# Kernel optimization log

Measured on AMD Instinct MI355X. Metric: run time of the kernel, lower is better.

## Reference

```python
import jax, jax.numpy as jnp
import numpy as np


def setup_inputs() -> dict:
    key = jax.random.key(0)
    k1, k2, k3 = jax.random.split(key, 3)
    b, c, h, w = 4, 124, 64, 64
    x = jax.random.normal(k1, (b, c, h, w), dtype=jnp.float32)
    # 1x1 conv, no bias -> channel-mixing matrix [c_out, c_in]
    Wb = jax.random.normal(k2, (c, c), dtype=jnp.float32) * (1.0 / np.sqrt(c))
    gamma = jax.random.normal(k3, (1,), dtype=jnp.float32) * 0.1
    return {"x": x, "Wb": Wb, "gamma": gamma}


def reference(x, Wb, gamma):
    b, c, h, w = x.shape
    n = h * w
    xf = x.reshape(b, c, n)                      # [b, c, n]
    # NOTE: original code applies convB for B, C, and D (convC/convD unused)
    Bf = jnp.einsum('oc,bcn->bon', Wb, xf)       # [b, c, n]
    # S = softmax(B^T C, dim=last) -> [b, n, n]
    scores = jnp.einsum('bcm,bcn->bmn', Bf, Bf)
    S = jax.nn.softmax(scores, axis=2)
    # E = D @ S^T -> E[b,c,m] = sum_n D[b,c,n] * S[b,m,n]
    E = jnp.einsum('bcn,bmn->bcm', Bf, S).reshape(b, c, h, w)
    return gamma[0] * E + x
```

## Files before the change

kernel.cpp:

```cpp
#include <hip/hip_runtime.h>

typedef short short8 __attribute__((ext_vector_type(8)));
typedef short short4v __attribute__((ext_vector_type(4)));
typedef float floatx4 __attribute__((ext_vector_type(4)));

#define BB 4
#define CC 124
#define CP 128
#define NN 4096
#define NGRP 256
#define NG32 128
#define NSPLIT 4
#define KSPLIT (NN / NSPLIT)
#define TN 32
#define NCHUNK (KSPLIT / TN)
#define NBUF 4

static __device__ __forceinline__ unsigned short f2bf_fast(float f) {
    return (unsigned short)((__float_as_uint(f) + 0x8000u) >> 16);
}
static __device__ __forceinline__ float bf2f(unsigned short u) {
    return __uint_as_float(((unsigned int)u) << 16);
}
static __device__ __forceinline__ unsigned int pkbf(float a, float b) {
    unsigned int ua = __float_as_uint(a) + 0x8000u;
    unsigned int ub = __float_as_uint(b) + 0x8000u;
    return __builtin_amdgcn_perm(ub, ua, 0x07060302u);
}
union PK2 { short4v s; unsigned int u[2]; };
union PK8 { short8 s; unsigned int u[4]; };

#if defined(__has_builtin) && __has_builtin(__builtin_amdgcn_exp2f)
static __device__ __forceinline__ float exp2_raw(float x) {
    return __builtin_amdgcn_exp2f(x);
}
#else
static __device__ __forceinline__ float exp2_raw(float x) {
    float r;
    asm("v_exp_f32 %0, %1\n\ts_nop 0" : "=v"(r) : "v"(x));
    return r;
}
#endif

static __device__ __forceinline__ void gl16(const unsigned short* g, unsigned short* l) {
    __builtin_amdgcn_global_load_lds(
        (const __attribute__((address_space(1))) unsigned int*)g,
        (__attribute__((address_space(3))) unsigned int*)l, 16, 0, 0);
}

__global__ __launch_bounds__(256) void wtrans_kernel(const float* __restrict__ Wb,
                                                     unsigned short* __restrict__ wbt) {
    __shared__ float ws[32][125];
    const int blk = blockIdx.x;
    const int tid = threadIdx.x;
    for (int i = tid; i < 32 * CC; i += 256) {
        int ol = i / CC, c = i - ol * CC;
        int o = blk * 32 + ol;
        ws[ol][c] = (o < CC) ? Wb[o * CC + c] : 0.f;
    }
    __syncthreads();
    for (int i = tid; i < CC * 32; i += 256) {
        int c = i >> 5, ol = i & 31;
        wbt[c * CP + blk * 32 + ol] = f2bf_fast(ws[ol][c]);
    }
}

__global__ __launch_bounds__(256, 4) void bf_proj_kernel(const float* __restrict__ x,
                                                         const unsigned short* __restrict__ wbt,
                                                         unsigned short* __restrict__ kfrag,
                                                         unsigned short* __restrict__ vfrag,
                                                         float* __restrict__ m2) {
    __shared__ __align__(16) float xs[CC][36];
    __shared__ float msh[32][33];
    const int tid = threadIdx.x;
    const int b = blockIdx.y;
    const int n0 = blockIdx.x * 32;
    const float* xb = x + (size_t)b * CC * NN + n0;
    for (int i = tid; i < CC * 8; i += 256) {
        int c = i >> 3, nq = i & 7;
        *(floatx4*)&xs[c][nq * 4] = *(const floatx4*)(xb + (size_t)c * NN + nq * 4);
    }
    __syncthreads();
    const int og = tid >> 3;
    const int nidx = tid & 7;
    const int o0 = og * 4;
    float acc[4][4];
#pragma unroll
    for (int k = 0; k < 4; ++k)
#pragma unroll
        for (int j = 0; j < 4; ++j) acc[k][j] = 0.f;
    for (int c = 0; c < CC; ++c) {
        floatx4 xv = *(const floatx4*)&xs[c][nidx * 4];
        short4v wv = *(const short4v*)&wbt[c * CP + o0];
#pragma unroll
        for (int k = 0; k < 4; ++k) {
            float wf = bf2f((unsigned short)wv[k]);
            acc[k][0] += wf * xv[0];
            acc[k][1] += wf * xv[1];
            acc[k][2] += wf * xv[2];
            acc[k][3] += wf * xv[3];
        }
    }
    float sq[4] = {0.f, 0.f, 0.f, 0.f};
#pragma unroll
    for (int k = 0; k < 4; ++k)
#pragma unroll
        for (int j = 0; j < 4; ++j) sq[j] += acc[k][j] * acc[k][j];
#pragma unroll
    for (int j = 0; j < 4; ++j) msh[og][nidx * 4 + j] = sq[j];
    const int g16 = (n0 >> 4) + (nidx & 1);
    const int tK = o0 >> 5;
    const int qK = (o0 >> 3) & 3;
    const int halfo = o0 & 7;
#pragma unroll
    for (int j = 0; j < 4; ++j) {
        PK2 kv;
        kv.u[0] = pkbf(acc[0][j], acc[1][j]);
        kv.u[1] = pkbf(acc[2][j], acc[3][j]);
        int row16 = 4 * (nidx >> 1) + j;
        size_t unit = ((size_t)(b * NGRP + g16) * 4 + tK) * 64 + qK * 16 + row16;
        *(short4v*)&kfrag[unit * 8 + halfo] = kv.s;
    }
    const int g32 = n0 >> 5;
    const int quadn = nidx >> 1;
    const int halfn = (nidx & 1) * 4;
#pragma unroll
    for (int k = 0; k < 4; ++k) {
        int c = o0 + k;
        PK2 vv;
        if (c == 124) {
            vv.u[0] = 0x3f803f80u;
            vv.u[1] = 0x3f803f80u;
        } else {
            vv.u[0] = pkbf(acc[k][0], acc[k][1]);
            vv.u[1] = pkbf(acc[k][2], acc[k][3]);
        }
        size_t unit = ((size_t)(b * NG32 + g32) * 8 + (c >> 4)) * 64 + quadn * 16 + (c & 15);
        *(short4v*)&vfrag[unit * 8 + halfn] = vv.s;
    }
    __syncthreads();
    if (tid < 32) {
        float s = 0.f;
#pragma unroll
        for (int og2 = 0; og2 < 32; ++og2) s += msh[og2][tid];
        m2[(size_t)b * NN + n0 + tid] = s * 1.44269504088896340736f;
    }
}

__global__ __launch_bounds__(256, 2) void attn_kernel(const unsigned short* __restrict__ kfrag,
                                                      const unsigned short* __restrict__ vfrag,
                                                      const float* __restrict__ m2,
                                                      unsigned short* __restrict__ opart) {
    __shared__ __align__(16) unsigned short kbuf[NBUF][8 * 512];
    __shared__ __align__(16) unsigned short vbuf[NBUF][8 * 512];
    const int id = blockIdx.x;
    const int ghi = id & 7;
    const int r_ = id >> 3;
    const int mtile = r_ & 31;
    const int glo = r_ >> 5;
    const int grp = ghi * 2 + glo;
    const int b = grp & 3;
    const int split = grp >> 2;
    const int w = threadIdx.x >> 6;
    const int lane = threadIdx.x & 63;
    const int col = lane & 15;
    const int quad = lane >> 4;
    const int m0 = mtile * 128 + w * 32;
    const floatx4 fzero = {0.f, 0.f, 0.f, 0.f};
    const float L2E = 1.44269504088896340736f;

    short8 qf[2][4];
#pragma unroll
    for (int ms = 0; ms < 2; ++ms) {
        const int gq = (m0 >> 4) + ms;
#pragma unroll
        for (int t = 0; t < 4; ++t)
            qf[ms][t] = *(const short8*)&kfrag[((size_t)(b * NGRP + gq) * 4 + t) * 512 + lane * 8];
    }
    const int mq = 8 * (col >> 2) + (col & 3);
    float nmreg[2];
    nmreg[0] = -m2[(size_t)b * NN + m0 + mq];
    nmreg[1] = -m2[(size_t)b * NN + m0 + mq + 4];

    floatx4 oacc[2][8];
#pragma unroll
    for (int ms = 0; ms < 2; ++ms)
#pragma unroll
        for (int s8 = 0; s8 < 8; ++s8) oacc[ms][s8] = fzero;

    auto stage = [&](int ch, int sel) {
        if (w < 2) {
            const int g16b = split * (KSPLIT >> 4) + ch * 2;
#pragma unroll
            for (int i = 0; i < 4; ++i) {
                int p = w * 4 + i;
                const unsigned short* src =
                    kfrag + ((size_t)(b * NGRP + g16b + (p >> 2)) * 4 + (p & 3)) * 512 + lane * 8;
                gl16(src, &kbuf[sel][p * 512]);
            }
        } else {
            const int g32b = split * (KSPLIT >> 5) + ch;
#pragma unroll
            for (int i = 0; i < 4; ++i) {
                int q = (w - 2) * 4 + i;
                const unsigned short* src =
                    vfrag + ((size_t)(b * NG32 + g32b) * 8 + q) * 512 + lane * 8;
                gl16(src, &vbuf[sel][q * 512]);
            }
        }
    };

    stage(0, 0);
    stage(1, 1);
    stage(2, 2);
    for (int ch = 0; ch < NCHUNK; ++ch) {
        if (ch + 2 < NCHUNK)      asm volatile("s_waitcnt vmcnt(8)" ::: "memory");
        else if (ch + 1 < NCHUNK) asm volatile("s_waitcnt vmcnt(4)" ::: "memory");
        else                      asm volatile("s_waitcnt vmcnt(0)" ::: "memory");
        __builtin_amdgcn_s_barrier();
        asm volatile("" ::: "memory");
        if (ch + 3 < NCHUNK) stage(ch + 3, (ch + 3) & (NBUF - 1));
        const int sel = ch & (NBUF - 1);
        floatx4 st[2][2];
#pragma unroll
        for (int ms = 0; ms < 2; ++ms)
#pragma unroll
            for (int u = 0; u < 2; ++u) st[ms][u] = fzero;
#pragma unroll
        for (int t = 0; t < 4; ++t) {
#pragma unroll
            for (int u = 0; u < 2; ++u) {
                short8 kf = *(const short8*)&kbuf[sel][((u * 4 + t) * 64 + lane) * 8];
                st[0][u] = __builtin_amdgcn_mfma_f32_16x16x32_bf16(kf, qf[0][t], st[0][u], 0, 0, 0);
                st[1][u] = __builtin_amdgcn_mfma_f32_16x16x32_bf16(kf, qf[1][t], st[1][u], 0, 0, 0);
            }
        }
        float ev[2][2][4];
#pragma unroll
        for (int ms = 0; ms < 2; ++ms)
#pragma unroll
            for (int u = 0; u < 2; ++u)
#pragma unroll
                for (int r = 0; r < 4; ++r)
                    ev[ms][u][r] = exp2_raw(__builtin_fmaf(st[ms][u][r], L2E, nmreg[ms]));
        PK8 af[2];
#pragma unroll
        for (int ms = 0; ms < 2; ++ms) {
            af[ms].u[0] = pkbf(ev[ms][0][0], ev[ms][0][1]);
            af[ms].u[1] = pkbf(ev[ms][0][2], ev[ms][0][3]);
            af[ms].u[2] = pkbf(ev[ms][1][0], ev[ms][1][1]);
            af[ms].u[3] = pkbf(ev[ms][1][2], ev[ms][1][3]);
        }
#pragma unroll
        for (int s8 = 0; s8 < 8; ++s8) {
            short8 vf = *(const short8*)&vbuf[sel][(s8 * 64 + lane) * 8];
            oacc[0][s8] = __builtin_amdgcn_mfma_f32_16x16x32_bf16(af[0].s, vf, oacc[0][s8], 0, 0, 0);
            oacc[1][s8] = __builtin_amdgcn_mfma_f32_16x16x32_bf16(af[1].s, vf, oacc[1][s8], 0, 0, 0);
        }
    }
    unsigned short* ob = opart + (size_t)(split * BB + b) * NN * CP;
#pragma unroll
    for (int ms = 0; ms < 2; ++ms)
#pragma unroll
        for (int s8 = 0; s8 < 8; ++s8)
#pragma unroll
            for (int r = 0; r < 4; ++r)
                ob[(size_t)(m0 + 8 * quad + 4 * ms + r) * CP + s8 * 16 + col] = f2bf_fast(oacc[ms][s8][r]);
}

__global__ __launch_bounds__(256) void combine_kernel(const unsigned short* __restrict__ opart,
                                                      const float* __restrict__ x,
                                                      const float* __restrict__ gamma,
                                                      float* __restrict__ out) {
    __shared__ float es[32 * 133];
    __shared__ float Lsh[32];
    const int t = threadIdx.x;
    const int b = blockIdx.y;
    const int m0 = blockIdx.x * 32;
    if (t < 32) {
        float L = 0.f;
#pragma unroll
        for (int s = 0; s < NSPLIT; ++s)
            L += bf2f(opart[((size_t)(s * BB + b) * NN + m0 + t) * CP + 124]);
        Lsh[t] = gamma[0] / L;
    }
    const int tc = t & 31, tm = t >> 5;
    float acc[4][4];
#pragma unroll
    for (int i = 0; i < 4; ++i)
#pragma unroll
        for (int j = 0; j < 4; ++j) acc[i][j] = 0.f;
    for (int s = 0; s < NSPLIT; ++s) {
        const unsigned short* obp = opart + ((size_t)(s * BB + b) * NN + m0 + tm * 4) * CP + tc * 4;
#pragma unroll
        for (int i = 0; i < 4; ++i) {
            short4v v = *(const short4v*)(obp + (size_t)i * CP);
            acc[i][0] += bf2f((unsigned short)v[0]);
            acc[i][1] += bf2f((unsigned short)v[1]);
            acc[i][2] += bf2f((unsigned short)v[2]);
            acc[i][3] += bf2f((unsigned short)v[3]);
        }
    }
#pragma unroll
    for (int i = 0; i < 4; ++i)
#pragma unroll
        for (int j = 0; j < 4; ++j) es[(tm * 4 + i) * 133 + tc * 4 + j] = acc[i][j];
    __syncthreads();
    const int wave = t >> 6, lane = t & 63;
    const int half = lane >> 5, lm = lane & 31;
#pragma unroll
    for (int p = 0; p < 16; ++p) {
        int c = p * 8 + wave * 2 + half;
        if (c < CC) {
            size_t base = ((size_t)b * CC + c) * NN + m0 + lm;
            out[base] = es[lm * 133 + c] * Lsh[lm] + x[base];
        }
    }
}

extern "C" void kernel_launch(void* const* d_in, const int* in_sizes, int n_in,
                              void* d_out, int out_size, void* d_ws, size_t ws_size,
                              hipStream_t stream) {
    const float* x = (const float*)d_in[0];
    const float* Wb = (const float*)d_in[1];
    const float* gamma = (const float*)d_in[2];
    float* out = (float*)d_out;

    const size_t kfrag_b = (size_t)BB * NGRP * 4 * 64 * 8 * sizeof(unsigned short);
    const size_t vfrag_b = (size_t)BB * NG32 * 8 * 64 * 8 * sizeof(unsigned short);
    const size_t m2_b = (size_t)BB * NN * sizeof(float);
    const size_t opart_b = (size_t)NSPLIT * BB * NN * CP * sizeof(unsigned short);
    const size_t wbt_b = (size_t)CC * CP * sizeof(unsigned short);
    if (ws_size < kfrag_b + vfrag_b + m2_b + opart_b + wbt_b) return;

    char* w = (char*)d_ws;
    unsigned short* kfrag = (unsigned short*)w;
    unsigned short* vfrag = (unsigned short*)(w + kfrag_b);
    float* m2 = (float*)(w + kfrag_b + vfrag_b);
    unsigned short* opart = (unsigned short*)(w + kfrag_b + vfrag_b + m2_b);
    unsigned short* wbt = (unsigned short*)(w + kfrag_b + vfrag_b + m2_b + opart_b);

    wtrans_kernel<<<dim3(4), 256, 0, stream>>>(Wb, wbt);
    bf_proj_kernel<<<dim3(NN / 32, BB), 256, 0, stream>>>(x, wbt, kfrag, vfrag, m2);
    attn_kernel<<<dim3(512), 256, 0, stream>>>(kfrag, vfrag, m2, opart);
    combine_kernel<<<dim3(NN / 32, BB), 256, 0, stream>>>(opart, x, gamma, out);
}
```

Measured before the change: 126.4 us.

## Software-pipeline PV MFMAs one chunk behind QK and split K/V prefetch depth

The loop now issues the PV matrix multiplies for the previous chunk right after the current chunk's QK multiplies, inside a raised-priority region. The exp and bf16 packing of the current scores can then overlap with matrix-core work instead of stalling it. K-loading waves prefetch three chunks ahead and V-loading waves two, with buffer indices rotated so the V tile stays live one extra iteration. A final epilogue drains the last chunk. This raises register pressure (af is carried across iterations) and adds an unroll-by-4 hint.

```diff
diff --git a/kernel.cpp b/kernel.cpp
--- a/kernel.cpp
+++ b/kernel.cpp
@@ -188,44 +188,50 @@
 #pragma unroll
         for (int s8 = 0; s8 < 8; ++s8) oacc[ms][s8] = fzero;
 
-    auto stage = [&](int ch, int sel) {
-        if (w < 2) {
-            const int g16b = split * (KSPLIT >> 4) + ch * 2;
-#pragma unroll
-            for (int i = 0; i < 4; ++i) {
-                int p = w * 4 + i;
-                const unsigned short* src =
-                    kfrag + ((size_t)(b * NGRP + g16b + (p >> 2)) * 4 + (p & 3)) * 512 + lane * 8;
-                gl16(src, &kbuf[sel][p * 512]);
-            }
-        } else {
-            const int g32b = split * (KSPLIT >> 5) + ch;
-#pragma unroll
-            for (int i = 0; i < 4; ++i) {
-                int q = (w - 2) * 4 + i;
-                const unsigned short* src =
-                    vfrag + ((size_t)(b * NG32 + g32b) * 8 + q) * 512 + lane * 8;
-                gl16(src, &vbuf[sel][q * 512]);
-            }
+    auto stageK = [&](int ch) {
+        const int sel = ch & (NBUF - 1);
+        const int g16b = split * (KSPLIT >> 4) + ch * 2;
+#pragma unroll
+        for (int i = 0; i < 4; ++i) {
+            int p = w * 4 + i;
+            const unsigned short* src =
+                kfrag + ((size_t)(b * NGRP + g16b + (p >> 2)) * 4 + (p & 3)) * 512 + lane * 8;
+            gl16(src, &kbuf[sel][p * 512]);
         }
     };
-
-    stage(0, 0);
-    stage(1, 1);
-    stage(2, 2);
+    auto stageV = [&](int ch) {
+        const int sel = ch & (NBUF - 1);
+        const int g32b = split * (KSPLIT >> 5) + ch;
+#pragma unroll
+        for (int i = 0; i < 4; ++i) {
+            int q = (w - 2) * 4 + i;
+            const unsigned short* src =
+                vfrag + ((size_t)(b * NG32 + g32b) * 8 + q) * 512 + lane * 8;
+            gl16(src, &vbuf[sel][q * 512]);
+        }
+    };
+
+    if (w < 2) { stageK(0); stageK(1); stageK(2); }
+    else       { stageV(0); stageV(1); }
+
+    PK8 af[2];
+#pragma unroll 4
     for (int ch = 0; ch < NCHUNK; ++ch) {
         if (ch + 2 < NCHUNK)      asm volatile("s_waitcnt vmcnt(8)" ::: "memory");
         else if (ch + 1 < NCHUNK) asm volatile("s_waitcnt vmcnt(4)" ::: "memory");
         else                      asm volatile("s_waitcnt vmcnt(0)" ::: "memory");
         __builtin_amdgcn_s_barrier();
         asm volatile("" ::: "memory");
-        if (ch + 3 < NCHUNK) stage(ch + 3, (ch + 3) & (NBUF - 1));
+        if (w < 2) { if (ch + 3 < NCHUNK) stageK(ch + 3); }
+        else       { if (ch + 2 < NCHUNK) stageV(ch + 2); }
         const int sel = ch & (NBUF - 1);
+        const int vsel = (ch - 1) & (NBUF - 1);
         floatx4 st[2][2];
 #pragma unroll
         for (int ms = 0; ms < 2; ++ms)
 #pragma unroll
             for (int u = 0; u < 2; ++u) st[ms][u] = fzero;
+        __builtin_amdgcn_s_setprio(1);
 #pragma unroll
         for (int t = 0; t < 4; ++t) {
 #pragma unroll
@@ -235,6 +241,15 @@
                 st[1][u] = __builtin_amdgcn_mfma_f32_16x16x32_bf16(kf, qf[1][t], st[1][u], 0, 0, 0);
             }
         }
+        if (ch > 0) {
+#pragma unroll
+            for (int s8 = 0; s8 < 8; ++s8) {
+                short8 vf = *(const short8*)&vbuf[vsel][(s8 * 64 + lane) * 8];
+                oacc[0][s8] = __builtin_amdgcn_mfma_f32_16x16x32_bf16(af[0].s, vf, oacc[0][s8], 0, 0, 0);
+                oacc[1][s8] = __builtin_amdgcn_mfma_f32_16x16x32_bf16(af[1].s, vf, oacc[1][s8], 0, 0, 0);
+            }
+        }
+        __builtin_amdgcn_s_setprio(0);
         float ev[2][2][4];
 #pragma unroll
         for (int ms = 0; ms < 2; ++ms)
@@ -243,7 +258,6 @@
 #pragma unroll
                 for (int r = 0; r < 4; ++r)
                     ev[ms][u][r] = exp2_raw(__builtin_fmaf(st[ms][u][r], L2E, nmreg[ms]));
-        PK8 af[2];
 #pragma unroll
         for (int ms = 0; ms < 2; ++ms) {
             af[ms].u[0] = pkbf(ev[ms][0][0], ev[ms][0][1]);
@@ -251,9 +265,12 @@
             af[ms].u[2] = pkbf(ev[ms][1][0], ev[ms][1][1]);
             af[ms].u[3] = pkbf(ev[ms][1][2], ev[ms][1][3]);
         }
+    }
+    {
+        const int vsel = (NCHUNK - 1) & (NBUF - 1);
 #pragma unroll
         for (int s8 = 0; s8 < 8; ++s8) {
-            short8 vf = *(const short8*)&vbuf[sel][(s8 * 64 + lane) * 8];
+            short8 vf = *(const short8*)&vbuf[vsel][(s8 * 64 + lane) * 8];
             oacc[0][s8] = __builtin_amdgcn_mfma_f32_16x16x32_bf16(af[0].s, vf, oacc[0][s8], 0, 0, 0);
             oacc[1][s8] = __builtin_amdgcn_mfma_f32_16x16x32_bf16(af[1].s, vf, oacc[1][s8], 0, 0, 0);
         }
```

After: 125.8 us. About the same (-0.4%).

## Load V directly into registers and skew PV MFMAs behind next QK

Applied to the files above, without the earlier changes.

Removes the LDS staging buffer for V. Each wave now loads its V fragments straight from global memory into registers, while K alone is staged in LDS, with each wave issuing two K loads. The loop is software-pipelined so the P·V MFMAs of the previous chunk are issued right after the QK MFMAs of the current chunk, ahead of the exp/pack work, with s_setprio raised around the MFMA block. The aim is to overlap the softmax exponent math with matrix work and to cut LDS traffic and barriers. In exchange, every wave reads the full V tile from global/L2, which quadruples V read traffic per block, and the two V register sets add VGPR pressure under the 2-blocks-per-CU bound.

```diff
diff --git a/kernel.cpp b/kernel.cpp
--- a/kernel.cpp
+++ b/kernel.cpp
@@ -147,12 +147,60 @@
     }
 }
 
+#define ATTN_WINDOW(CH, VC, VP, DO_PV)                                             \
+    {                                                                              \
+        _Pragma("unroll")                                                          \
+        for (int s8_ = 0; s8_ < 8; ++s8_)                                          \
+            VC[s8_] = *(const short8*)(vbase + (size_t)((CH) * 8 + s8_) * 512);    \
+        if ((CH) + 3 < NCHUNK) stageK((CH) + 3);                                   \
+        const int sel_ = (CH) & (NBUF - 1);                                        \
+        floatx4 st[2][2];                                                          \
+        _Pragma("unroll")                                                          \
+        for (int ms_ = 0; ms_ < 2; ++ms_)                                          \
+            _Pragma("unroll")                                                      \
+            for (int u_ = 0; u_ < 2; ++u_) st[ms_][u_] = fzero;                    \
+        __builtin_amdgcn_s_setprio(1);                                             \
+        _Pragma("unroll")                                                          \
+        for (int t_ = 0; t_ < 4; ++t_) {                                           \
+            _Pragma("unroll")                                                      \
+            for (int u_ = 0; u_ < 2; ++u_) {                                       \
+                short8 kf_ = *(const short8*)&kbuf[sel_][((u_ * 4 + t_) * 64 + lane) * 8]; \
+                st[0][u_] = __builtin_amdgcn_mfma_f32_16x16x32_bf16(kf_, qf[0][t_], st[0][u_], 0, 0, 0); \
+                st[1][u_] = __builtin_amdgcn_mfma_f32_16x16x32_bf16(kf_, qf[1][t_], st[1][u_], 0, 0, 0); \
+            }                                                                      \
+        }                                                                          \
+        if (DO_PV) {                                                               \
+            _Pragma("unroll")                                                      \
+            for (int s8_ = 0; s8_ < 8; ++s8_) {                                    \
+                oacc[0][s8_] = __builtin_amdgcn_mfma_f32_16x16x32_bf16(af[0].s, VP[s8_], oacc[0][s8_], 0, 0, 0); \
+                oacc[1][s8_] = __builtin_amdgcn_mfma_f32_16x16x32_bf16(af[1].s, VP[s8_], oacc[1][s8_], 0, 0, 0); \
+            }                                                                      \
+        }                                                                          \
+        __builtin_amdgcn_s_setprio(0);                                             \
+        float ev[2][2][4];                                                         \
+        _Pragma("unroll")                                                          \
+        for (int ms_ = 0; ms_ < 2; ++ms_)                                          \
+            _Pragma("unroll")                                                      \
+            for (int u_ = 0; u_ < 2; ++u_)                                         \
+                _Pragma("unroll")                                                  \
+                for (int r_2 = 0; r_2 < 4; ++r_2)                                  \
+                    ev[ms_][u_][r_2] = exp2_raw(__builtin_fmaf(st[ms_][u_][r_2], L2E, nmreg[ms_])); \
+        _Pragma("unroll")                                                          \
+        for (int ms_ = 0; ms_ < 2; ++ms_) {                                        \
+            af[ms_].u[0] = pkbf(ev[ms_][0][0], ev[ms_][0][1]);                     \
+            af[ms_].u[1] = pkbf(ev[ms_][0][2], ev[ms_][0][3]);                     \
+            af[ms_].u[2] = pkbf(ev[ms_][1][0], ev[ms_][1][1]);                     \
+            af[ms_].u[3] = pkbf(ev[ms_][1][2], ev[ms_][1][3]);                     \
+        }                                                                          \
+        asm volatile("s_waitcnt vmcnt(10)" ::: "memory");                          \
+        __builtin_amdgcn_s_barrier();                                              \
+    }
+
 __global__ __launch_bounds__(256, 2) void attn_kernel(const unsigned short* __restrict__ kfrag,
                                                       const unsigned short* __restrict__ vfrag,
                                                       const float* __restrict__ m2,
                                                       unsigned short* __restrict__ opart) {
     __shared__ __align__(16) unsigned short kbuf[NBUF][8 * 512];
-    __shared__ __align__(16) unsigned short vbuf[NBUF][8 * 512];
     const int id = blockIdx.x;
     const int ghi = id & 7;
     const int r_ = id >> 3;
@@ -188,75 +236,38 @@
 #pragma unroll
         for (int s8 = 0; s8 < 8; ++s8) oacc[ms][s8] = fzero;
 
-    auto stage = [&](int ch, int sel) {
-        if (w < 2) {
-            const int g16b = split * (KSPLIT >> 4) + ch * 2;
-#pragma unroll
-            for (int i = 0; i < 4; ++i) {
-                int p = w * 4 + i;
-                const unsigned short* src =
-                    kfrag + ((size_t)(b * NGRP + g16b + (p >> 2)) * 4 + (p & 3)) * 512 + lane * 8;
-                gl16(src, &kbuf[sel][p * 512]);
-            }
-        } else {
-            const int g32b = split * (KSPLIT >> 5) + ch;
-#pragma unroll
-            for (int i = 0; i < 4; ++i) {
-                int q = (w - 2) * 4 + i;
-                const unsigned short* src =
-                    vfrag + ((size_t)(b * NG32 + g32b) * 8 + q) * 512 + lane * 8;
-                gl16(src, &vbuf[sel][q * 512]);
-            }
+    const unsigned short* vbase =
+        vfrag + ((size_t)(b * NG32 + split * (KSPLIT >> 5)) * 8) * 512 + lane * 8;
+
+    auto stageK = [&](int ch) {
+        const int sel = ch & (NBUF - 1);
+        const int g16b = split * (KSPLIT >> 4) + ch * 2;
+#pragma unroll
+        for (int i = 0; i < 2; ++i) {
+            int p = w * 2 + i;
+            const unsigned short* src =
+                kfrag + ((size_t)(b * NGRP + g16b + (p >> 2)) * 4 + (p & 3)) * 512 + lane * 8;
+            gl16(src, &kbuf[sel][p * 512]);
         }
     };
 
-    stage(0, 0);
-    stage(1, 1);
-    stage(2, 2);
-    for (int ch = 0; ch < NCHUNK; ++ch) {
-        if (ch + 2 < NCHUNK)      asm volatile("s_waitcnt vmcnt(8)" ::: "memory");
-        else if (ch + 1 < NCHUNK) asm volatile("s_waitcnt vmcnt(4)" ::: "memory");
-        else                      asm volatile("s_waitcnt vmcnt(0)" ::: "memory");
-        __builtin_amdgcn_s_barrier();
-        asm volatile("" ::: "memory");
-        if (ch + 3 < NCHUNK) stage(ch + 3, (ch + 3) & (NBUF - 1));
-        const int sel = ch & (NBUF - 1);
-        floatx4 st[2][2];
-#pragma unroll
-        for (int ms = 0; ms < 2; ++ms)
-#pragma unroll
-            for (int u = 0; u < 2; ++u) st[ms][u] = fzero;
-#pragma unroll
-        for (int t = 0; t < 4; ++t) {
-#pragma unroll
-            for (int u = 0; u < 2; ++u) {
-                short8 kf = *(const short8*)&kbuf[sel][((u * 4 + t) * 64 + lane) * 8];
-                st[0][u] = __builtin_amdgcn_mfma_f32_16x16x32_bf16(kf, qf[0][t], st[0][u], 0, 0, 0);
-                st[1][u] = __builtin_amdgcn_mfma_f32_16x16x32_bf16(kf, qf[1][t], st[1][u], 0, 0, 0);
-            }
-        }
-        float ev[2][2][4];
-#pragma unroll
-        for (int ms = 0; ms < 2; ++ms)
-#pragma unroll
-            for (int u = 0; u < 2; ++u)
-#pragma unroll
-                for (int r = 0; r < 4; ++r)
-                    ev[ms][u][r] = exp2_raw(__builtin_fmaf(st[ms][u][r], L2E, nmreg[ms]));
-        PK8 af[2];
-#pragma unroll
-        for (int ms = 0; ms < 2; ++ms) {
-            af[ms].u[0] = pkbf(ev[ms][0][0], ev[ms][0][1]);
-            af[ms].u[1] = pkbf(ev[ms][0][2], ev[ms][0][3]);
-            af[ms].u[2] = pkbf(ev[ms][1][0], ev[ms][1][1]);
-            af[ms].u[3] = pkbf(ev[ms][1][2], ev[ms][1][3]);
-        }
-#pragma unroll
-        for (int s8 = 0; s8 < 8; ++s8) {
-            short8 vf = *(const short8*)&vbuf[sel][(s8 * 64 + lane) * 8];
-            oacc[0][s8] = __builtin_amdgcn_mfma_f32_16x16x32_bf16(af[0].s, vf, oacc[0][s8], 0, 0, 0);
-            oacc[1][s8] = __builtin_amdgcn_mfma_f32_16x16x32_bf16(af[1].s, vf, oacc[1][s8], 0, 0, 0);
-        }
+    stageK(0); stageK(1); stageK(2);
+    asm volatile("s_waitcnt vmcnt(4)" ::: "memory");
+    __builtin_amdgcn_s_barrier();
+
+    short8 VA[8], VB[8];
+    PK8 af[2];
+    ATTN_WINDOW(0, VA, VB, 0)
+    ATTN_WINDOW(1, VB, VA, 1)
+#pragma unroll 1
+    for (int chp = 2; chp < NCHUNK; chp += 2) {
+        ATTN_WINDOW(chp, VA, VB, 1)
+        ATTN_WINDOW(chp + 1, VB, VA, 1)
+    }
+#pragma unroll
+    for (int s8 = 0; s8 < 8; ++s8) {
+        oacc[0][s8] = __builtin_amdgcn_mfma_f32_16x16x32_bf16(af[0].s, VB[s8], oacc[0][s8], 0, 0, 0);
+        oacc[1][s8] = __builtin_amdgcn_mfma_f32_16x16x32_bf16(af[1].s, VB[s8], oacc[1][s8], 0, 0, 0);
     }
     unsigned short* ob = opart + (size_t)(split * BB + b) * NN * CP;
 #pragma unroll
```

Result: slower. 131.3 us (+3.9%).
